# Optimization experiments

Hardware: AMD Instinct MI355X
Metric: run time of the kernel (lower is better)

The kernel has to match this reference:

```python
import jax, jax.numpy as jnp
import numpy as np

NEG_INF = -9e15
ALPHA = 0.2  # leaky relu slope


def setup_inputs() -> dict:
    key = jax.random.key(0)
    k1, k2, k3, k4 = jax.random.split(key, 4)
    B, N, Din = 8, 1024, 128
    H, D = 8, 16
    h = jax.random.normal(k1, (B, N, Din), dtype=jnp.float32)
    adj = jax.random.randint(k2, (B, N, N), 0, 2, dtype=jnp.int32)
    W = jax.random.normal(k3, (Din, H * D), dtype=jnp.float32) * 0.1
    a = jax.random.normal(k4, (H, 2 * D, 1), dtype=jnp.float32) * 0.1
    return {"h": h, "adj": adj, "W": W, "a": a}


def reference(h, adj, W, a):
    B, N, _ = h.shape
    H, twoD, _ = a.shape
    D = twoD // 2
    # Wh: [B, N, H, D]
    Wh = (h @ W).reshape(B, N, H, D)
    # Decompose additive attention: a . [Wh_i ; Wh_j] = a_src . Wh_i + a_dst . Wh_j
    a_src = a[:, :D, 0]   # [H, D]
    a_dst = a[:, D:, 0]   # [H, D]
    s_i = jnp.einsum('bnhd,hd->bhn', Wh, a_src)  # [B, H, N]
    s_j = jnp.einsum('bnhd,hd->bhn', Wh, a_dst)  # [B, H, N]
    scores = jax.nn.leaky_relu(s_i[:, :, :, None] + s_j[:, :, None, :], ALPHA)  # [B,H,N,N]
    scores = jnp.where(adj[:, None, :, :] == 0, NEG_INF, scores)
    attn = jax.nn.softmax(scores, axis=-1)  # [B, H, N, N]
    # Weighted aggregation over neighbors j
    h_prime = jnp.einsum('bhij,bjhd->bihd', attn, Wh).reshape(B, N, H * D)
    return h_prime
```

## Files before the change

kernel.cpp:

```cpp
#include <hip/hip_runtime.h>
#include <hip/hip_bf16.h>

constexpr int B   = 8;
constexpr int N   = 1024;
constexpr int DIN = 128;
constexpr int H   = 8;
constexpr int D   = 16;
constexpr int HD  = 128;
constexpr int TI  = 16;

#define LOG2E 1.4426950408889634f
#define TCLAMP 30.0f

typedef __attribute__((ext_vector_type(8))) short bf16x8;
typedef __attribute__((ext_vector_type(4))) float f32x4;

__device__ inline float fast_exp2(float x) {
#if __has_builtin(__builtin_amdgcn_exp2f)
    return __builtin_amdgcn_exp2f(x);
#else
    return exp2f(x);
#endif
}

__global__ __launch_bounds__(256) void k_pack(const int* __restrict__ adj,
                                              unsigned int* __restrict__ bm)
{
    const size_t g = (size_t)blockIdx.x * 256 + threadIdx.x;
    const unsigned long long m = __ballot(adj[g] != 0);
    const int l = threadIdx.x & 63;
    if (l == 0)  bm[g >> 5] = (unsigned int)m;
    if (l == 32) bm[g >> 5] = (unsigned int)(m >> 32);
}

__global__ __launch_bounds__(256) void k_proj(
    const float* __restrict__ hsrc,
    const float* __restrict__ W,
    const float* __restrict__ a,
    __hip_bfloat16* __restrict__ WhT,
    float* __restrict__ tI,
    float* __restrict__ tJ)
{
    const int row0 = blockIdx.x * 32;
    const int b    = row0 >> 10;
    const int n0   = row0 & (N - 1);
    const int t    = threadIdx.x;
    const int lane = t & 63, wave = t >> 6;
    const int mn   = lane & 15, kg = lane >> 4;

    __shared__ __align__(16) __hip_bfloat16 hA[32][136];
    __shared__ __align__(16) __hip_bfloat16 Wt[128][136];

    {
        const float4* hf = reinterpret_cast<const float4*>(hsrc + (size_t)row0 * DIN);
        #pragma unroll
        for (int u = 0; u < 4; ++u) {
            const int idx = t + u * 256;
            const float4 v = hf[idx];
            const int r = idx >> 5, c4 = (idx & 31) * 4;
            hA[r][c4]     = __float2bfloat16(v.x);
            hA[r][c4 + 1] = __float2bfloat16(v.y);
            hA[r][c4 + 2] = __float2bfloat16(v.z);
            hA[r][c4 + 3] = __float2bfloat16(v.w);
        }
    }
    {
        const float4* wf = reinterpret_cast<const float4*>(W);
        #pragma unroll
        for (int u = 0; u < 16; ++u) {
            const int idx = t + u * 256;
            const float4 v = wf[idx];
            const int k = idx >> 5, c0 = (idx & 31) * 4;
            Wt[c0][k]     = __float2bfloat16(v.x);
            Wt[c0 + 1][k] = __float2bfloat16(v.y);
            Wt[c0 + 2][k] = __float2bfloat16(v.z);
            Wt[c0 + 3][k] = __float2bfloat16(v.w);
        }
    }
    __syncthreads();

    const int lr0 = (wave >> 1) * 16;
    const int ch  = wave & 1;
    f32x4 acc[4];
    #pragma unroll
    for (int f = 0; f < 4; ++f) acc[f] = (f32x4){0.f, 0.f, 0.f, 0.f};

    #pragma unroll
    for (int kk = 0; kk < 4; ++kk) {
        const bf16x8 af = *reinterpret_cast<const bf16x8*>(
            &hA[lr0 + mn][kk * 32 + kg * 8]);
        #pragma unroll
        for (int f = 0; f < 4; ++f) {
            const bf16x8 bf = *reinterpret_cast<const bf16x8*>(
                &Wt[ch * 64 + f * 16 + mn][kk * 32 + kg * 8]);
            acc[f] = __builtin_amdgcn_mfma_f32_16x16x32_bf16(af, bf, acc[f], 0, 0, 0);
        }
    }

    #pragma unroll
    for (int f = 0; f < 4; ++f) {
        const int hh = ch * 4 + f;
        const float as = a[hh * 32 + mn];
        const float ad = a[hh * 32 + 16 + mn];
        #pragma unroll
        for (int r = 0; r < 4; ++r) {
            const int n = n0 + lr0 + kg * 4 + r;
            WhT[((size_t)(b * HD + ch * 64 + f * 16 + mn)) * N + n] =
                __float2bfloat16(acc[f][r]);
            float vi = acc[f][r] * as;
            float vj = acc[f][r] * ad;
            #pragma unroll
            for (int m = 1; m < 16; m <<= 1) {
                vi += __shfl_xor(vi, m);
                vj += __shfl_xor(vj, m);
            }
            if (mn == 0) {
                tI[((size_t)(b * H + hh)) * N + n] = fminf(vi * LOG2E, TCLAMP);
                tJ[((size_t)(b * H + hh)) * N + n] = fminf(vj * LOG2E, TCLAMP);
            }
        }
    }
}

__global__ __launch_bounds__(256, 4) void k_attn(
    const unsigned int*   __restrict__ bm,
    const __hip_bfloat16* __restrict__ WhT,
    const float*          __restrict__ tI,
    const float*          __restrict__ tJ,
    float*                __restrict__ out)
{
    const int b    = blockIdx.y;
    const int i0   = blockIdx.x * TI;
    const int lane = threadIdx.x & 63;
    const int h    = blockIdx.z * 4 + (threadIdx.x >> 6);
    const int mn   = lane & 15, kg = lane >> 4;
    const int row  = i0 + mn;

    const float Arow = tI[((size_t)(b * H + h)) * N + row];
    const float* tjrow = tJ + ((size_t)(b * H + h)) * N + kg * 8;
    const __hip_bfloat16* wrow =
        WhT + ((size_t)(b * HD + h * 16 + mn)) * N + kg * 8;
    const uint4* mrow = reinterpret_cast<const uint4*>(
        bm + ((size_t)(b * N) + row) * 32);

    f32x4 accO = {0.f, 0.f, 0.f, 0.f};
    f32x4 accD = {0.f, 0.f, 0.f, 0.f};
    bf16x8 ones;
    #pragma unroll
    for (int e = 0; e < 8; ++e) ones[e] = (short)0x3F80;

    for (int sq = 0; sq < 8; ++sq) {
        const int j0 = sq * 128;

        const uint4 mv4 = mrow[sq];
        float4 ta[4], tb[4]; bf16x8 wv[4];
        #pragma unroll
        for (int q = 0; q < 4; ++q) {
            ta[q] = *reinterpret_cast<const float4*>(tjrow + j0 + q * 32);
            tb[q] = *reinterpret_cast<const float4*>(tjrow + j0 + q * 32 + 4);
            wv[q] = *reinterpret_cast<const bf16x8*>(wrow + j0 + q * 32);
        }
        const unsigned int mvq[4] = {mv4.x, mv4.y, mv4.z, mv4.w};

        #pragma unroll
        for (int q = 0; q < 4; ++q) {
            const unsigned int m8 = (mvq[q] >> (kg * 8)) & 0xFFu;
            const float tv[8] = {ta[q].x, ta[q].y, ta[q].z, ta[q].w,
                                 tb[q].x, tb[q].y, tb[q].z, tb[q].w};
            bf16x8 af;
            #pragma unroll
            for (int e = 0; e < 8; ++e) {
                const float x = Arow + tv[e];
                float sc = fmaxf(x, 0.2f * x);
                sc = ((m8 >> e) & 1u) ? sc : -1.0e30f;
                af[e] = (short)__bfloat16_as_ushort(
                    __float2bfloat16(fast_exp2(sc)));
            }
            accO = __builtin_amdgcn_mfma_f32_16x16x32_bf16(af, wv[q], accO, 0, 0, 0);
            accD = __builtin_amdgcn_mfma_f32_16x16x32_bf16(af, ones, accD, 0, 0, 0);
        }
    }

    #pragma unroll
    for (int r = 0; r < 4; ++r) {
        out[((size_t)(b * N) + i0 + kg * 4 + r) * HD + h * 16 + mn] =
            accO[r] / accD[r];
    }
}

extern "C" void kernel_launch(void* const* d_in, const int* in_sizes, int n_in,
                              void* d_out, int out_size, void* d_ws, size_t ws_size,
                              hipStream_t stream)
{
    const float* h   = (const float*)d_in[0];
    const int*   adj = (const int*)d_in[1];
    const float* W   = (const float*)d_in[2];
    const float* a   = (const float*)d_in[3];
    float* out = (float*)d_out;

    float* ws = (float*)d_ws;
    float* tI = ws;
    float* tJ = ws + (size_t)B * H * N;
    __hip_bfloat16* WhT = (__hip_bfloat16*)(ws + (size_t)2 * B * H * N);
    unsigned int* bm = (unsigned int*)((char*)WhT +
                       (size_t)B * N * HD * sizeof(__hip_bfloat16));

    k_pack<<<dim3((B * N * N) / 256), dim3(256), 0, stream>>>(adj, bm);
    k_proj<<<dim3(B * N / 32), dim3(256), 0, stream>>>(h, W, a, WhT, tI, tJ);
    k_attn<<<dim3(N / TI, B, 2), dim3(256), 0, stream>>>(bm, WhT, tI, tJ, out);
}
```

Baseline: 55.16 us.

## Fuse adjacency bitmask packing into attention kernel and cover all heads per block

Removes the separate pack kernel: each attention block now ballots its own 16 rows of the int32 adjacency into a shared-memory bitmask, so the adjacency is read once without a round trip through a global bitmask. The attention block grows to 512 threads covering all 8 heads, so the packed mask is shared across heads and each row of adj is read once rather than twice. The projection kernel is also split into 16-row blocks to get more blocks. This saves a kernel launch and the bitmask write and read, at the cost of a larger block and a sync before compute.

```diff
diff --git a/kernel.cpp b/kernel.cpp
--- a/kernel.cpp
+++ b/kernel.cpp
@@ -21,16 +21,6 @@
 #else
     return exp2f(x);
 #endif
-}
-
-__global__ __launch_bounds__(256) void k_pack(const int* __restrict__ adj,
-                                              unsigned int* __restrict__ bm)
-{
-    const size_t g = (size_t)blockIdx.x * 256 + threadIdx.x;
-    const unsigned long long m = __ballot(adj[g] != 0);
-    const int l = threadIdx.x & 63;
-    if (l == 0)  bm[g >> 5] = (unsigned int)m;
-    if (l == 32) bm[g >> 5] = (unsigned int)(m >> 32);
 }
 
 __global__ __launch_bounds__(256) void k_proj(
@@ -41,20 +31,20 @@
     float* __restrict__ tI,
     float* __restrict__ tJ)
 {
-    const int row0 = blockIdx.x * 32;
+    const int row0 = blockIdx.x * 16;
     const int b    = row0 >> 10;
     const int n0   = row0 & (N - 1);
     const int t    = threadIdx.x;
     const int lane = t & 63, wave = t >> 6;
     const int mn   = lane & 15, kg = lane >> 4;
 
-    __shared__ __align__(16) __hip_bfloat16 hA[32][136];
+    __shared__ __align__(16) __hip_bfloat16 hA[16][136];
     __shared__ __align__(16) __hip_bfloat16 Wt[128][136];
 
     {
         const float4* hf = reinterpret_cast<const float4*>(hsrc + (size_t)row0 * DIN);
         #pragma unroll
-        for (int u = 0; u < 4; ++u) {
+        for (int u = 0; u < 2; ++u) {
             const int idx = t + u * 256;
             const float4 v = hf[idx];
             const int r = idx >> 5, c4 = (idx & 31) * 4;
@@ -79,33 +69,32 @@
     }
     __syncthreads();
 
-    const int lr0 = (wave >> 1) * 16;
-    const int ch  = wave & 1;
-    f32x4 acc[4];
-    #pragma unroll
-    for (int f = 0; f < 4; ++f) acc[f] = (f32x4){0.f, 0.f, 0.f, 0.f};
+    f32x4 acc[2];
+    acc[0] = (f32x4){0.f, 0.f, 0.f, 0.f};
+    acc[1] = (f32x4){0.f, 0.f, 0.f, 0.f};
 
     #pragma unroll
     for (int kk = 0; kk < 4; ++kk) {
         const bf16x8 af = *reinterpret_cast<const bf16x8*>(
-            &hA[lr0 + mn][kk * 32 + kg * 8]);
-        #pragma unroll
-        for (int f = 0; f < 4; ++f) {
-            const bf16x8 bf = *reinterpret_cast<const bf16x8*>(
-                &Wt[ch * 64 + f * 16 + mn][kk * 32 + kg * 8]);
-            acc[f] = __builtin_amdgcn_mfma_f32_16x16x32_bf16(af, bf, acc[f], 0, 0, 0);
-        }
-    }
-
-    #pragma unroll
-    for (int f = 0; f < 4; ++f) {
-        const int hh = ch * 4 + f;
-        const float as = a[hh * 32 + mn];
-        const float ad = a[hh * 32 + 16 + mn];
+            &hA[mn][kk * 32 + kg * 8]);
+        #pragma unroll
+        for (int f = 0; f < 2; ++f) {
+            const int F = wave * 2 + f;
+            const bf16x8 bfr = *reinterpret_cast<const bf16x8*>(
+                &Wt[F * 16 + mn][kk * 32 + kg * 8]);
+            acc[f] = __builtin_amdgcn_mfma_f32_16x16x32_bf16(af, bfr, acc[f], 0, 0, 0);
+        }
+    }
+
+    #pragma unroll
+    for (int f = 0; f < 2; ++f) {
+        const int F = wave * 2 + f;
+        const float as = a[F * 32 + mn];
+        const float ad = a[F * 32 + 16 + mn];
         #pragma unroll
         for (int r = 0; r < 4; ++r) {
-            const int n = n0 + lr0 + kg * 4 + r;
-            WhT[((size_t)(b * HD + ch * 64 + f * 16 + mn)) * N + n] =
+            const int n = n0 + kg * 4 + r;
+            WhT[((size_t)(b * HD + F * 16 + mn)) * N + n] =
                 __float2bfloat16(acc[f][r]);
             float vi = acc[f][r] * as;
             float vj = acc[f][r] * ad;
@@ -115,15 +104,15 @@
                 vj += __shfl_xor(vj, m);
             }
             if (mn == 0) {
-                tI[((size_t)(b * H + hh)) * N + n] = fminf(vi * LOG2E, TCLAMP);
-                tJ[((size_t)(b * H + hh)) * N + n] = fminf(vj * LOG2E, TCLAMP);
-            }
-        }
-    }
-}
-
-__global__ __launch_bounds__(256, 4) void k_attn(
-    const unsigned int*   __restrict__ bm,
+                tI[((size_t)(b * H + F)) * N + n] = fminf(vi * LOG2E, TCLAMP);
+                tJ[((size_t)(b * H + F)) * N + n] = fminf(vj * LOG2E, TCLAMP);
+            }
+        }
+    }
+}
+
+__global__ __launch_bounds__(512, 4) void k_attn(
+    const int*            __restrict__ adj,
     const __hip_bfloat16* __restrict__ WhT,
     const float*          __restrict__ tI,
     const float*          __restrict__ tJ,
@@ -131,17 +120,33 @@
 {
     const int b    = blockIdx.y;
     const int i0   = blockIdx.x * TI;
-    const int lane = threadIdx.x & 63;
-    const int h    = blockIdx.z * 4 + (threadIdx.x >> 6);
+    const int t    = threadIdx.x;
+    const int lane = t & 63, h = t >> 6;
     const int mn   = lane & 15, kg = lane >> 4;
-    const int row  = i0 + mn;
-
-    const float Arow = tI[((size_t)(b * H + h)) * N + row];
+
+    __shared__ unsigned int m2[32][16];
+
+    {
+        const int* ar = adj + ((size_t)(b * N) + i0 + 2 * h) * N + lane;
+        #pragma unroll
+        for (int rr = 0; rr < 2; ++rr) {
+            #pragma unroll
+            for (int tt = 0; tt < 16; ++tt) {
+                const int v = ar[rr * N + tt * 64];
+                const unsigned long long mm = __ballot(v != 0);
+                if (lane == 0)
+                    m2[2 * tt][2 * h + rr] = (unsigned int)mm;
+                if (lane == 32)
+                    m2[2 * tt + 1][2 * h + rr] = (unsigned int)(mm >> 32);
+            }
+        }
+    }
+    __syncthreads();
+
+    const float Arow = tI[((size_t)(b * H + h)) * N + i0 + mn];
     const float* tjrow = tJ + ((size_t)(b * H + h)) * N + kg * 8;
     const __hip_bfloat16* wrow =
         WhT + ((size_t)(b * HD + h * 16 + mn)) * N + kg * 8;
-    const uint4* mrow = reinterpret_cast<const uint4*>(
-        bm + ((size_t)(b * N) + row) * 32);
 
     f32x4 accO = {0.f, 0.f, 0.f, 0.f};
     f32x4 accD = {0.f, 0.f, 0.f, 0.f};
@@ -152,7 +157,9 @@
     for (int sq = 0; sq < 8; ++sq) {
         const int j0 = sq * 128;
 
-        const uint4 mv4 = mrow[sq];
+        unsigned int mvq[4];
+        #pragma unroll
+        for (int q = 0; q < 4; ++q) mvq[q] = m2[sq * 4 + q][mn];
         float4 ta[4], tb[4]; bf16x8 wv[4];
         #pragma unroll
         for (int q = 0; q < 4; ++q) {
@@ -160,7 +167,6 @@
             tb[q] = *reinterpret_cast<const float4*>(tjrow + j0 + q * 32 + 4);
             wv[q] = *reinterpret_cast<const bf16x8*>(wrow + j0 + q * 32);
         }
-        const unsigned int mvq[4] = {mv4.x, mv4.y, mv4.z, mv4.w};
 
         #pragma unroll
         for (int q = 0; q < 4; ++q) {
@@ -202,10 +208,7 @@
     float* tI = ws;
     float* tJ = ws + (size_t)B * H * N;
     __hip_bfloat16* WhT = (__hip_bfloat16*)(ws + (size_t)2 * B * H * N);
-    unsigned int* bm = (unsigned int*)((char*)WhT +
-                       (size_t)B * N * HD * sizeof(__hip_bfloat16));
-
-    k_pack<<<dim3((B * N * N) / 256), dim3(256), 0, stream>>>(adj, bm);
-    k_proj<<<dim3(B * N / 32), dim3(256), 0, stream>>>(h, W, a, WhT, tI, tJ);
-    k_attn<<<dim3(N / TI, B, 2), dim3(256), 0, stream>>>(bm, WhT, tI, tJ, out);
-}
+
+    k_proj<<<dim3(B * N / 16), dim3(256), 0, stream>>>(h, W, a, WhT, tI, tJ);
+    k_attn<<<dim3(N / TI, B), dim3(512), 0, stream>>>(adj, WhT, tI, tJ, out);
+}
```

Result: no change. 55.10 us (-0.1%).
